# Performance work log

Measured on AMD Instinct MI355X. Metric: run time of the kernel, lower is better.

The kernel has to match this reference:

```python
import jax, jax.numpy as jnp
import numpy as np

B, H, W, N, DX, DZ = 4, 64, 64, 4096, 2, 128
INIT_LS = 0.1


def setup_inputs() -> dict:
    key = jax.random.key(0)
    k1, k2, k3, k4 = jax.random.split(key, 4)
    xc_off_grid = jax.random.uniform(k1, (B, N, DX), dtype=jnp.float32)
    # regular grid coordinates in [0, 1]^2, broadcast over batch
    gy, gx = jnp.meshgrid(jnp.linspace(0.0, 1.0, H), jnp.linspace(0.0, 1.0, W), indexing="ij")
    xc_on_grid = jnp.broadcast_to(jnp.stack([gy, gx], axis=-1)[None], (B, H, W, DX)).astype(jnp.float32)
    zc_off_grid = jax.random.normal(k2, (B, N, DZ), dtype=jnp.float32)
    zc_on_grid = jax.random.normal(k3, (B, H, W, DZ), dtype=jnp.float32)
    # lengthscale_param = log(exp(init_lengthscale) - 1)  (inverse softplus)
    lengthscale_param = jnp.log(jnp.expm1(jnp.full((DX,), INIT_LS, dtype=jnp.float32)))
    return {
        "xc_off_grid": xc_off_grid,
        "xc_on_grid": xc_on_grid,
        "zc_off_grid": zc_off_grid,
        "zc_on_grid": zc_on_grid,
        "lengthscale_param": lengthscale_param,
        "ignore_on_grid": 0,
    }


def reference(xc_off_grid, xc_on_grid, zc_off_grid, zc_on_grid, lengthscale_param, ignore_on_grid):
    b = xc_on_grid.shape[0]
    grid_shape = xc_on_grid.shape[1:-1]
    dz = zc_off_grid.shape[-1]
    xg = xc_on_grid.reshape(b, -1, xc_on_grid.shape[-1])  # [b, m, dx]
    lengthscale = 1e-05 + jax.nn.softplus(lengthscale_param)  # [dx]
    # squared scaled distances: [b, m, n]
    diff = (xg[:, :, None, :] - xc_off_grid[:, None, :, :]) / lengthscale
    weights = jnp.exp(-0.5 * jnp.sum(diff * diff, axis=-1))  # [b, m, n]
    zc = jnp.einsum("bmn,bnd->bmd", weights, zc_off_grid)  # [b, m, dz]
    if not ignore_on_grid:
        zc = zc + zc_on_grid.reshape(b, -1, dz)
    return zc.reshape((b,) + grid_shape + (dz,))
```

## Files before the change

kernel.cpp:

```cpp
#include <hip/hip_runtime.h>

#define HH 64
#define WW 64
#define NN 4096
#define DZc 128
#define KS 8
#define BK 64
#define NKT (NN / KS / BK)
#define CELLS 2097152
#define ZT_BYTES (4ull * 128 * 4096 * 2ull)
#define WS_NEED (ZT_BYTES + 8ull * CELLS * 2ull)

typedef __fp16 v2fp16 __attribute__((ext_vector_type(2)));
typedef _Float16 v4h __attribute__((ext_vector_type(4)));
typedef _Float16 v8h __attribute__((ext_vector_type(8)));
typedef float v16f __attribute__((ext_vector_type(16)));
typedef double v2d __attribute__((ext_vector_type(2)));

__device__ __forceinline__ unsigned pk16(float lo, float hi){
  union { v2fp16 h; unsigned u; } c;
  c.h = __builtin_amdgcn_cvt_pkrtz(lo, hi);
  return c.u;
}
__device__ __forceinline__ float fexp2(float x){ return __builtin_amdgcn_exp2f(x); }

__global__ __launch_bounds__(256, 8)
void init_out_kernel(const float4* __restrict__ zc_on,
                     const int* __restrict__ ignore,
                     float4* __restrict__ out){
  int i = blockIdx.x * blockDim.x + threadIdx.x;
  float4 v = zc_on[i];
  if (ignore[0]) { v.x = 0.f; v.y = 0.f; v.z = 0.f; v.w = 0.f; }
  out[i] = v;
}

__global__ __launch_bounds__(256, 4)
void prepack_kernel(const float* __restrict__ zc_off, _Float16* __restrict__ zt_g){
  __shared__ unsigned tt[128 * 34];
  const int bidx = blockIdx.x;
  const int b  = bidx >> 6;
  const int n0 = (bidx & 63) * 64;
  const int t  = threadIdx.x;

  const int np = t >> 3;
  const int d0 = (t & 7) * 16;
  const float* r0 = zc_off + ((size_t)(b * NN + n0 + 2 * np)) * DZc + d0;
  float4 a[4], c[4];
  #pragma unroll
  for (int i = 0; i < 4; ++i){
    a[i] = *(const float4*)&r0[4 * i];
    c[i] = *(const float4*)&r0[DZc + 4 * i];
  }
  const float* af = (const float*)a;
  const float* cf = (const float*)c;
  #pragma unroll
  for (int j = 0; j < 16; ++j)
    tt[(d0 + j) * 34 + np] = pk16(af[j], cf[j]);

  __syncthreads();

  const int d  = t >> 1;
  const int nh = t & 1;
  const unsigned* rr = tt + d * 34 + nh * 16;
  _Float16* w = zt_g + ((size_t)(b * DZc + d)) * NN + n0 + nh * 32;
  double v[8];
  #pragma unroll
  for (int j = 0; j < 8; ++j) v[j] = *(const double*)&rr[2 * j];
  #pragma unroll
  for (int j = 0; j < 4; ++j){
    v2d s; s[0] = v[2 * j]; s[1] = v[2 * j + 1];
    *(v2d*)&w[8 * j] = s;
  }
}

__global__ __launch_bounds__(256, 8)
void reduce_kernel(const v8h* __restrict__ part,
                   const float4* __restrict__ zc_on,
                   const int* __restrict__ ignore,
                   float4* __restrict__ out){
  int i = blockIdx.x * blockDim.x + threadIdx.x;
  float4 s0 = zc_on[2 * i];
  float4 s1 = zc_on[2 * i + 1];
  if (ignore[0]) {
    s0.x = s0.y = s0.z = s0.w = 0.f;
    s1.x = s1.y = s1.z = s1.w = 0.f;
  }
  #pragma unroll
  for (int ks = 0; ks < KS; ++ks){
    v8h p = part[(size_t)ks * (CELLS / 8) + i];
    s0.x += (float)p[0]; s0.y += (float)p[1]; s0.z += (float)p[2]; s0.w += (float)p[3];
    s1.x += (float)p[4]; s1.y += (float)p[5]; s1.z += (float)p[6]; s1.w += (float)p[7];
  }
  out[2 * i]     = s0;
  out[2 * i + 1] = s1;
}

template<bool PRE>
__global__ __launch_bounds__(256, 2)
void setconv_gemm_kernel(const float* __restrict__ xc_off,
                         const float* __restrict__ xc_on,
                         const float* __restrict__ zc_off,
                         const _Float16* __restrict__ zpack,
                         const float* __restrict__ lsp,
                         _Float16* __restrict__ part,
                         float* __restrict__ out)
{
  __shared__ unsigned short zt[2][128][68];
  __shared__ unsigned short gt[2][40][72];

  const int tid = threadIdx.x;
  const int bid = blockIdx.x;
  const int ks  = bid >> 6;
  const int bm  = bid & 63;
  const int b   = bm >> 4;
  const int mt  = bm & 15;
  const int iy0 = (mt >> 3) * 32;
  const int ix0 = (mt & 7) * 8;
  const int nbase = ks * (NN / KS);

  const float lsy = 1e-5f + log1pf(expf(lsp[0]));
  const float lsx = 1e-5f + log1pf(expf(lsp[1]));
  const float LOG2E = 1.44269504088896340736f;
  const float ay = -0.5f * LOG2E / (lsy * lsy);
  const float ax = -0.5f * LOG2E / (lsx * lsx);

  const int gp = tid & 31;
  const int gr = tid >> 5;
  float gc[5], ga[5];
  #pragma unroll
  for (int i = 0; i < 5; ++i){
    int row = gr + 8 * i;
    if (row < 32){ gc[i] = xc_on[((b * HH + iy0 + row) * WW) * 2];        ga[i] = ay; }
    else         { gc[i] = xc_on[(b * HH * WW + ix0 + row - 32) * 2 + 1]; ga[i] = ax; }
  }

  const int zd  = (tid & 63) | (((tid >> 6) & 1) << 6);
  const int zkh = tid >> 7;
  const _Float16* ztg = PRE ? (zpack + ((size_t)(b * DZc + zd)) * NN + nbase + zkh * 32)
                            : (const _Float16*)nullptr;

  const int lane = tid & 63;
  const int wv  = tid >> 6;
  const int l31 = lane & 31;
  const int lh  = lane >> 5;
  const int gxr = 32 + (l31 & 7);
  const int gyr = wv * 8 + (l31 >> 3);

  v16f acc[2][4];
  #pragma unroll
  for (int m = 0; m < 2; ++m)
    #pragma unroll
    for (int d = 0; d < 4; ++d)
      #pragma unroll
      for (int r = 0; r < 16; ++r)
        acc[m][d][r] = 0.f;

  const float* xb = xc_off + (size_t)b * NN * 2;
  const float* zb = zc_off + (size_t)b * NN * DZc;

  {
    const int n0 = nbase;
    float4 xq = *(const float4*)&xb[(size_t)(n0 + 2 * gp) * 2];
    unsigned* gw = (unsigned*)&gt[0][0][0];
    #pragma unroll
    for (int i = 0; i < 5; ++i){
      int row = gr + 8 * i;
      float s0 = (row < 32) ? xq.x : xq.y;
      float s1 = (row < 32) ? xq.z : xq.w;
      float d0 = gc[i] - s0, d1 = gc[i] - s1;
      gw[row * 36 + gp] = pk16(fexp2(ga[i] * d0 * d0), fexp2(ga[i] * d1 * d1));
    }
    if (PRE){
      #pragma unroll
      for (int i = 0; i < 4; ++i){
        union { v8h v; double d[2]; } u;
        u.v = *(const v8h*)&ztg[8 * i];
        *(double*)&zt[0][zd][zkh * 32 + 8 * i]     = u.d[0];
        *(double*)&zt[0][zd][zkh * 32 + 8 * i + 4] = u.d[1];
      }
    } else {
      float zv[32];
      #pragma unroll
      for (int i = 0; i < 32; ++i)
        zv[i] = zb[(size_t)(n0 + zkh * 32 + i) * DZc + zd];
      #pragma unroll
      for (int j = 0; j < 8; ++j){
        union { unsigned u[2]; double d; } w;
        w.u[0] = pk16(zv[4 * j],     zv[4 * j + 1]);
        w.u[1] = pk16(zv[4 * j + 2], zv[4 * j + 3]);
        *(double*)&zt[0][zd][zkh * 32 + 4 * j] = w.d;
      }
    }
  }
  __syncthreads();

  #pragma unroll 1
  for (int kt = 0; kt < NKT; ++kt){
    const int buf  = kt & 1;
    const int nbuf = buf ^ 1;
    const bool have_next = (kt + 1 < NKT);
    const int n1 = nbase + (kt + 1) * BK;

    v8h zrn[4];
    float zv[32];
    float4 xq_n = (float4){0.f, 0.f, 0.f, 0.f};
    if (have_next){
      if (PRE){
        #pragma unroll
        for (int i = 0; i < 4; ++i)
          zrn[i] = *(const v8h*)&ztg[(kt + 1) * BK + 8 * i];
      } else {
        #pragma unroll
        for (int i = 0; i < 32; ++i)
          zv[i] = zb[(size_t)(n1 + zkh * 32 + i) * DZc + zd];
      }
      xq_n = *(const float4*)&xb[(size_t)(n1 + 2 * gp) * 2];
    }

    __builtin_amdgcn_s_setprio(1);
    #pragma unroll
    for (int kstep = 0; kstep < 4; ++kstep){
      const int k0 = kstep * 16 + lh * 8;
      const v8h xu = *(const v8h*)&gt[buf][gxr][k0];
      v8h bfr[4];
      #pragma unroll
      for (int dtl = 0; dtl < 4; ++dtl){
        union { v4h h[2]; v8h v; } zu;
        zu.h[0] = *(const v4h*)&zt[buf][dtl * 32 + l31][k0];
        zu.h[1] = *(const v4h*)&zt[buf][dtl * 32 + l31][k0 + 4];
        bfr[dtl] = zu.v;
      }
      #pragma unroll
      for (int mtl = 0; mtl < 2; ++mtl){
        const v8h yu = *(const v8h*)&gt[buf][gyr + mtl * 4][k0];
        v8h av = yu * xu;
        #pragma unroll
        for (int dtl = 0; dtl < 4; ++dtl)
          acc[mtl][dtl] = __builtin_amdgcn_mfma_f32_32x32x16_f16(av, bfr[dtl], acc[mtl][dtl], 0, 0, 0);
      }
    }
    __builtin_amdgcn_s_setprio(0);

    if (have_next){
      if (PRE){
        #pragma unroll
        for (int i = 0; i < 4; ++i){
          union { v8h v; double d[2]; } u;
          u.v = zrn[i];
          *(double*)&zt[nbuf][zd][zkh * 32 + 8 * i]     = u.d[0];
          *(double*)&zt[nbuf][zd][zkh * 32 + 8 * i + 4] = u.d[1];
        }
      } else {
        #pragma unroll
        for (int j = 0; j < 8; ++j){
          union { unsigned u[2]; double d; } w;
          w.u[0] = pk16(zv[4 * j],     zv[4 * j + 1]);
          w.u[1] = pk16(zv[4 * j + 2], zv[4 * j + 3]);
          *(double*)&zt[nbuf][zd][zkh * 32 + 4 * j] = w.d;
        }
      }
      unsigned* gw = (unsigned*)&gt[nbuf][0][0];
      #pragma unroll
      for (int i = 0; i < 5; ++i){
        int row = gr + 8 * i;
        float s0 = (row < 32) ? xq_n.x : xq_n.y;
        float s1 = (row < 32) ? xq_n.z : xq_n.w;
        float d0 = gc[i] - s0, d1 = gc[i] - s1;
        gw[row * 36 + gp] = pk16(fexp2(ga[i] * d0 * d0), fexp2(ga[i] * d1 * d1));
      }
    }
    __syncthreads();
  }

  if (part){
    _Float16* pw = part + (size_t)ks * CELLS;
    #pragma unroll
    for (int mtl = 0; mtl < 2; ++mtl)
      #pragma unroll
      for (int dtl = 0; dtl < 4; ++dtl){
        const int d = dtl * 32 + l31;
        #pragma unroll
        for (int reg = 0; reg < 16; ++reg){
          const int row = (reg & 3) + 8 * (reg >> 2) + 4 * lh;
          const int m = wv * 64 + mtl * 32 + row;
          const int iy = iy0 + (m >> 3);
          const int ix = ix0 + (m & 7);
          pw[((b * HH + iy) * WW + ix) * DZc + d] = (_Float16)acc[mtl][dtl][reg];
        }
      }
  } else {
    #pragma unroll
    for (int mtl = 0; mtl < 2; ++mtl)
      #pragma unroll
      for (int dtl = 0; dtl < 4; ++dtl){
        const int d = dtl * 32 + l31;
        #pragma unroll
        for (int reg = 0; reg < 16; ++reg){
          const int row = (reg & 3) + 8 * (reg >> 2) + 4 * lh;
          const int m = wv * 64 + mtl * 32 + row;
          const int iy = iy0 + (m >> 3);
          const int ix = ix0 + (m & 7);
          unsafeAtomicAdd(&out[((b * HH + iy) * WW + ix) * DZc + d], acc[mtl][dtl][reg]);
        }
      }
  }
}

extern "C" void kernel_launch(void* const* d_in, const int* in_sizes, int n_in,
                              void* d_out, int out_size, void* d_ws, size_t ws_size,
                              hipStream_t stream){
  const float* xc_off = (const float*)d_in[0];
  const float* xc_on  = (const float*)d_in[1];
  const float* zc_off = (const float*)d_in[2];
  const float* zc_on  = (const float*)d_in[3];
  const float* lsp    = (const float*)d_in[4];
  const int*   ign    = (const int*)d_in[5];
  float* out = (float*)d_out;

  if (ws_size >= WS_NEED){
    _Float16* zpack = (_Float16*)d_ws;
    _Float16* part  = (_Float16*)((char*)d_ws + ZT_BYTES);
    prepack_kernel<<<4 * 64, 256, 0, stream>>>(zc_off, zpack);
    setconv_gemm_kernel<true><<<KS * 64, 256, 0, stream>>>(xc_off, xc_on, zc_off, zpack, lsp, part, out);
    reduce_kernel<<<CELLS / 8 / 256, 256, 0, stream>>>((const v8h*)part, (const float4*)zc_on, ign, (float4*)out);
  } else {
    init_out_kernel<<<CELLS / 4 / 256, 256, 0, stream>>>((const float4*)zc_on, ign, (float4*)out);
    setconv_gemm_kernel<false><<<KS * 64, 256, 0, stream>>>(xc_off, xc_on, zc_off, nullptr, lsp, nullptr, out);
  }
}
```

Before: 106.9 us.

## Split GEMM block across 8 waves with halved per-wave DZ tile

Doubles the GEMM block from 256 to 512 threads. Each wave now covers half of the 128 output channels (2 d-tiles instead of 4), which halves the accumulator registers per wave. The loads that stage the weight rows and the z tiles are redistributed over the larger thread count. The aim is more waves in flight per CU to hide LDS and global latency, in exchange for fewer MFMAs per LDS fragment load and more threads taking part in each barrier.

```diff
diff --git a/kernel.cpp b/kernel.cpp
--- a/kernel.cpp
+++ b/kernel.cpp
@@ -96,7 +96,7 @@
 }
 
 template<bool PRE>
-__global__ __launch_bounds__(256, 2)
+__global__ __launch_bounds__(512, 4)
 void setconv_gemm_kernel(const float* __restrict__ xc_off,
                          const float* __restrict__ xc_on,
                          const float* __restrict__ zc_off,
@@ -126,31 +126,35 @@
 
   const int gp = tid & 31;
   const int gr = tid >> 5;
-  float gc[5], ga[5];
-  #pragma unroll
-  for (int i = 0; i < 5; ++i){
-    int row = gr + 8 * i;
-    if (row < 32){ gc[i] = xc_on[((b * HH + iy0 + row) * WW) * 2];        ga[i] = ay; }
-    else         { gc[i] = xc_on[(b * HH * WW + ix0 + row - 32) * 2 + 1]; ga[i] = ax; }
-  }
-
-  const int zd  = (tid & 63) | (((tid >> 6) & 1) << 6);
-  const int zkh = tid >> 7;
-  const _Float16* ztg = PRE ? (zpack + ((size_t)(b * DZc + zd)) * NN + nbase + zkh * 32)
+  float gc[3], ga[3];
+  #pragma unroll
+  for (int i = 0; i < 3; ++i){
+    int row = gr + 16 * i;
+    if (row < 32)      { gc[i] = xc_on[((b * HH + iy0 + row) * WW) * 2];        ga[i] = ay; }
+    else if (row < 40) { gc[i] = xc_on[(b * HH * WW + ix0 + row - 32) * 2 + 1]; ga[i] = ax; }
+    else               { gc[i] = 0.f; ga[i] = 0.f; }
+  }
+
+  const int zd = tid & 127;
+  const int zq = tid >> 7;
+  const _Float16* ztg = PRE ? (zpack + ((size_t)(b * DZc + zd)) * NN + nbase + zq * 16)
                             : (const _Float16*)nullptr;
 
   const int lane = tid & 63;
   const int wv  = tid >> 6;
+  const int mq  = wv >> 1;
+  const int dh  = wv & 1;
   const int l31 = lane & 31;
   const int lh  = lane >> 5;
   const int gxr = 32 + (l31 & 7);
-  const int gyr = wv * 8 + (l31 >> 3);
-
-  v16f acc[2][4];
+  const int gyr = mq * 8 + (l31 >> 3);
+  const int dbase = dh * 64;
+
+  v16f acc[2][2];
   #pragma unroll
   for (int m = 0; m < 2; ++m)
     #pragma unroll
-    for (int d = 0; d < 4; ++d)
+    for (int d = 0; d < 2; ++d)
       #pragma unroll
       for (int r = 0; r < 16; ++r)
         acc[m][d][r] = 0.f;
@@ -163,32 +167,34 @@
     float4 xq = *(const float4*)&xb[(size_t)(n0 + 2 * gp) * 2];
     unsigned* gw = (unsigned*)&gt[0][0][0];
     #pragma unroll
-    for (int i = 0; i < 5; ++i){
-      int row = gr + 8 * i;
-      float s0 = (row < 32) ? xq.x : xq.y;
-      float s1 = (row < 32) ? xq.z : xq.w;
-      float d0 = gc[i] - s0, d1 = gc[i] - s1;
-      gw[row * 36 + gp] = pk16(fexp2(ga[i] * d0 * d0), fexp2(ga[i] * d1 * d1));
+    for (int i = 0; i < 3; ++i){
+      int row = gr + 16 * i;
+      if (row < 40){
+        float s0 = (row < 32) ? xq.x : xq.y;
+        float s1 = (row < 32) ? xq.z : xq.w;
+        float d0 = gc[i] - s0, d1 = gc[i] - s1;
+        gw[row * 36 + gp] = pk16(fexp2(ga[i] * d0 * d0), fexp2(ga[i] * d1 * d1));
+      }
     }
     if (PRE){
       #pragma unroll
-      for (int i = 0; i < 4; ++i){
+      for (int i = 0; i < 2; ++i){
         union { v8h v; double d[2]; } u;
         u.v = *(const v8h*)&ztg[8 * i];
-        *(double*)&zt[0][zd][zkh * 32 + 8 * i]     = u.d[0];
-        *(double*)&zt[0][zd][zkh * 32 + 8 * i + 4] = u.d[1];
+        *(double*)&zt[0][zd][zq * 16 + 8 * i]     = u.d[0];
+        *(double*)&zt[0][zd][zq * 16 + 8 * i + 4] = u.d[1];
       }
     } else {
-      float zv[32];
-      #pragma unroll
-      for (int i = 0; i < 32; ++i)
-        zv[i] = zb[(size_t)(n0 + zkh * 32 + i) * DZc + zd];
-      #pragma unroll
-      for (int j = 0; j < 8; ++j){
+      float zv[16];
+      #pragma unroll
+      for (int i = 0; i < 16; ++i)
+        zv[i] = zb[(size_t)(n0 + zq * 16 + i) * DZc + zd];
+      #pragma unroll
+      for (int j = 0; j < 4; ++j){
         union { unsigned u[2]; double d; } w;
         w.u[0] = pk16(zv[4 * j],     zv[4 * j + 1]);
         w.u[1] = pk16(zv[4 * j + 2], zv[4 * j + 3]);
-        *(double*)&zt[0][zd][zkh * 32 + 4 * j] = w.d;
+        *(double*)&zt[0][zd][zq * 16 + 4 * j] = w.d;
       }
     }
   }
@@ -201,18 +207,18 @@
     const bool have_next = (kt + 1 < NKT);
     const int n1 = nbase + (kt + 1) * BK;
 
-    v8h zrn[4];
-    float zv[32];
+    v8h zrn[2];
+    float zv[16];
     float4 xq_n = (float4){0.f, 0.f, 0.f, 0.f};
     if (have_next){
       if (PRE){
         #pragma unroll
-        for (int i = 0; i < 4; ++i)
+        for (int i = 0; i < 2; ++i)
           zrn[i] = *(const v8h*)&ztg[(kt + 1) * BK + 8 * i];
       } else {
         #pragma unroll
-        for (int i = 0; i < 32; ++i)
-          zv[i] = zb[(size_t)(n1 + zkh * 32 + i) * DZc + zd];
+        for (int i = 0; i < 16; ++i)
+          zv[i] = zb[(size_t)(n1 + zq * 16 + i) * DZc + zd];
       }
       xq_n = *(const float4*)&xb[(size_t)(n1 + 2 * gp) * 2];
     }
@@ -222,12 +228,12 @@
     for (int kstep = 0; kstep < 4; ++kstep){
       const int k0 = kstep * 16 + lh * 8;
       const v8h xu = *(const v8h*)&gt[buf][gxr][k0];
-      v8h bfr[4];
-      #pragma unroll
-      for (int dtl = 0; dtl < 4; ++dtl){
+      v8h bfr[2];
+      #pragma unroll
+      for (int dtl = 0; dtl < 2; ++dtl){
         union { v4h h[2]; v8h v; } zu;
-        zu.h[0] = *(const v4h*)&zt[buf][dtl * 32 + l31][k0];
-        zu.h[1] = *(const v4h*)&zt[buf][dtl * 32 + l31][k0 + 4];
+        zu.h[0] = *(const v4h*)&zt[buf][dbase + dtl * 32 + l31][k0];
+        zu.h[1] = *(const v4h*)&zt[buf][dbase + dtl * 32 + l31][k0 + 4];
         bfr[dtl] = zu.v;
       }
       #pragma unroll
@@ -235,7 +241,7 @@
         const v8h yu = *(const v8h*)&gt[buf][gyr + mtl * 4][k0];
         v8h av = yu * xu;
         #pragma unroll
-        for (int dtl = 0; dtl < 4; ++dtl)
+        for (int dtl = 0; dtl < 2; ++dtl)
           acc[mtl][dtl] = __builtin_amdgcn_mfma_f32_32x32x16_f16(av, bfr[dtl], acc[mtl][dtl], 0, 0, 0);
       }
     }
@@ -244,29 +250,31 @@
     if (have_next){
       if (PRE){
         #pragma unroll
-        for (int i = 0; i < 4; ++i){
+        for (int i = 0; i < 2; ++i){
           union { v8h v; double d[2]; } u;
           u.v = zrn[i];
-          *(double*)&zt[nbuf][zd][zkh * 32 + 8 * i]     = u.d[0];
-          *(double*)&zt[nbuf][zd][zkh * 32 + 8 * i + 4] = u.d[1];
+          *(double*)&zt[nbuf][zd][zq * 16 + 8 * i]     = u.d[0];
+          *(double*)&zt[nbuf][zd][zq * 16 + 8 * i + 4] = u.d[1];
         }
       } else {
         #pragma unroll
-        for (int j = 0; j < 8; ++j){
+        for (int j = 0; j < 4; ++j){
           union { unsigned u[2]; double d; } w;
           w.u[0] = pk16(zv[4 * j],     zv[4 * j + 1]);
           w.u[1] = pk16(zv[4 * j + 2], zv[4 * j + 3]);
-          *(double*)&zt[nbuf][zd][zkh * 32 + 4 * j] = w.d;
+          *(double*)&zt[nbuf][zd][zq * 16 + 4 * j] = w.d;
         }
       }
       unsigned* gw = (unsigned*)&gt[nbuf][0][0];
       #pragma unroll
-      for (int i = 0; i < 5; ++i){
-        int row = gr + 8 * i;
-        float s0 = (row < 32) ? xq_n.x : xq_n.y;
-        float s1 = (row < 32) ? xq_n.z : xq_n.w;
-        float d0 = gc[i] - s0, d1 = gc[i] - s1;
-        gw[row * 36 + gp] = pk16(fexp2(ga[i] * d0 * d0), fexp2(ga[i] * d1 * d1));
+      for (int i = 0; i < 3; ++i){
+        int row = gr + 16 * i;
+        if (row < 40){
+          float s0 = (row < 32) ? xq_n.x : xq_n.y;
+          float s1 = (row < 32) ? xq_n.z : xq_n.w;
+          float d0 = gc[i] - s0, d1 = gc[i] - s1;
+          gw[row * 36 + gp] = pk16(fexp2(ga[i] * d0 * d0), fexp2(ga[i] * d1 * d1));
+        }
       }
     }
     __syncthreads();
@@ -277,12 +285,12 @@
     #pragma unroll
     for (int mtl = 0; mtl < 2; ++mtl)
       #pragma unroll
-      for (int dtl = 0; dtl < 4; ++dtl){
-        const int d = dtl * 32 + l31;
+      for (int dtl = 0; dtl < 2; ++dtl){
+        const int d = dbase + dtl * 32 + l31;
         #pragma unroll
         for (int reg = 0; reg < 16; ++reg){
           const int row = (reg & 3) + 8 * (reg >> 2) + 4 * lh;
-          const int m = wv * 64 + mtl * 32 + row;
+          const int m = mq * 64 + mtl * 32 + row;
           const int iy = iy0 + (m >> 3);
           const int ix = ix0 + (m & 7);
           pw[((b * HH + iy) * WW + ix) * DZc + d] = (_Float16)acc[mtl][dtl][reg];
@@ -292,12 +300,12 @@
     #pragma unroll
     for (int mtl = 0; mtl < 2; ++mtl)
       #pragma unroll
-      for (int dtl = 0; dtl < 4; ++dtl){
-        const int d = dtl * 32 + l31;
+      for (int dtl = 0; dtl < 2; ++dtl){
+        const int d = dbase + dtl * 32 + l31;
         #pragma unroll
         for (int reg = 0; reg < 16; ++reg){
           const int row = (reg & 3) + 8 * (reg >> 2) + 4 * lh;
-          const int m = wv * 64 + mtl * 32 + row;
+          const int m = mq * 64 + mtl * 32 + row;
           const int iy = iy0 + (m >> 3);
           const int ix = ix0 + (m & 7);
           unsafeAtomicAdd(&out[((b * HH + iy) * WW + ix) * DZc + d], acc[mtl][dtl][reg]);
@@ -321,10 +329,10 @@
     _Float16* zpack = (_Float16*)d_ws;
     _Float16* part  = (_Float16*)((char*)d_ws + ZT_BYTES);
     prepack_kernel<<<4 * 64, 256, 0, stream>>>(zc_off, zpack);
-    setconv_gemm_kernel<true><<<KS * 64, 256, 0, stream>>>(xc_off, xc_on, zc_off, zpack, lsp, part, out);
+    setconv_gemm_kernel<true><<<KS * 64, 512, 0, stream>>>(xc_off, xc_on, zc_off, zpack, lsp, part, out);
     reduce_kernel<<<CELLS / 8 / 256, 256, 0, stream>>>((const v8h*)part, (const float4*)zc_on, ign, (float4*)out);
   } else {
     init_out_kernel<<<CELLS / 4 / 256, 256, 0, stream>>>((const float4*)zc_on, ign, (float4*)out);
-    setconv_gemm_kernel<false><<<KS * 64, 256, 0, stream>>>(xc_off, xc_on, zc_off, nullptr, lsp, nullptr, out);
-  }
-}
+    setconv_gemm_kernel<false><<<KS * 64, 512, 0, stream>>>(xc_off, xc_on, zc_off, nullptr, lsp, nullptr, out);
+  }
+}
```

After: 105.2 us (median of 2 runs). Within noise of the previous version (-1.6%).
